# Kernel optimization log

Hardware: AMD Instinct MI355X
Metric: run time of the kernel (lower is better)

## Reference

```python
import jax, jax.numpy as jnp
import numpy as np

BN_EPS = 1e-5
B, N, D, E, L, VOCAB = 256, 256, 256, 262144, 5, 16
V = B * N


def batch_norm(h, g, b):
    # BatchNorm1d in training mode: biased batch stats over the node axis
    mu = jnp.mean(h, axis=0)
    var = jnp.mean((h - mu) ** 2, axis=0)
    return (h - mu) * jax.lax.rsqrt(var + BN_EPS) * g + b


def setup_inputs() -> dict:
    key = jax.random.key(0)
    ks = jax.random.split(key, 10)
    return {
        "x": jax.random.normal(ks[0], (B, N + 1, D), jnp.float32),
        "edge_weight": jax.random.uniform(ks[1], (E,), jnp.float32),
        "bond_emb": 0.02 * jax.random.normal(ks[2], (L, 3, VOCAB, D), jnp.float32),
        "W1": 0.02 * jax.random.normal(ks[3], (L, D, 2 * D), jnp.float32),
        "b1": jnp.zeros((L, 2 * D), jnp.float32),
        "bn1_g": jnp.ones((L, 2 * D), jnp.float32),
        "bn1_b": jnp.zeros((L, 2 * D), jnp.float32),
        "W2": 0.02 * jax.random.normal(ks[4], (L, 2 * D, D), jnp.float32),
        "b2": jnp.zeros((L, D), jnp.float32),
        "bn2_g": jnp.ones((L, D), jnp.float32),
        "bn2_b": jnp.zeros((L, D), jnp.float32),
        "eps_param": jnp.zeros((L,), jnp.float32),
        "x_mask": jnp.ones((B, N), jnp.int32),
        "edge_index": jax.random.randint(ks[5], (2, E), 0, V, jnp.int32),
        "edge_attr": jax.random.randint(ks[6], (E, 3), 0, VOCAB, jnp.int32),
    }


def reference(x, edge_weight, bond_emb, W1, b1, bn1_g, bn1_b, W2, b2,
              bn2_g, bn2_b, eps_param, x_mask, edge_index, edge_attr):
    res = x
    # mask is all-ones -> x[x_mask] equals the flattened [B*N, D] node tensor
    h = x[:, 1:, :].reshape(-1, D)
    mask = x_mask.reshape(-1).astype(x.dtype)[:, None]

    # add_self_loops: append (i, i) for every node; self-loop attr = [5, 7, 0]
    sl = jnp.arange(V, dtype=edge_index.dtype)
    src = jnp.concatenate([edge_index[0], sl])
    dst = jnp.concatenate([edge_index[1], sl])
    ea = jnp.concatenate(
        [edge_attr, jnp.broadcast_to(jnp.array([5, 7, 0], edge_attr.dtype), (V, 3))], axis=0)
    ew = jnp.concatenate([edge_weight, jnp.ones((V,), edge_weight.dtype)])

    for i in range(L):
        # BondEncoder: sum of per-feature embedding lookups -> [E+V, D]
        eemb = (bond_emb[i, 0][ea[:, 0]] + bond_emb[i, 1][ea[:, 1]]
                + bond_emb[i, 2][ea[:, 2]])
        msg = jax.nn.relu(h[src] + eemb) * ew[:, None]       # gather + relu
        aggr = jax.ops.segment_sum(msg, dst, num_segments=V)  # scatter-add
        z = (1.0 + eps_param[i]) * h + aggr
        z = batch_norm(z @ W1[i] + b1[i], bn1_g[i], bn1_b[i])
        z = jax.nn.relu(z) @ W2[i] + b2[i]
        z = batch_norm(z, bn2_g[i], bn2_b[i])                 # GNNBlock norm
        if i != L - 1:                                        # last_act
            z = jax.nn.relu(z)
        h = z                                                  # drop_ratio=0

    rep = h * mask  # x_zeros[x_mask] = node_representation (JK='last')
    return res.at[:, 1:, :].add(rep.reshape(res.shape[0], -1, D))
```

## Files before the change

kernel.cpp:

```cpp
#include <hip/hip_runtime.h>

#define E_EDGES 262144
#define V_NODES 65536
#define D_DIM   256

typedef short bf16x8 __attribute__((ext_vector_type(8)));
typedef float f32x4  __attribute__((ext_vector_type(4)));

__device__ __forceinline__ unsigned short f2bf(float f) {
  union { float f; unsigned u; } x; x.f = f;
  unsigned r = x.u + 0x7FFFu + ((x.u >> 16) & 1u);
  return (unsigned short)(r >> 16);
}
__device__ __forceinline__ float bf2f(unsigned short h) {
  union { unsigned u; float f; } x; x.u = ((unsigned)h) << 16;
  return x.f;
}
__device__ __forceinline__ void async16(const void* g, void* l) {
  __builtin_amdgcn_global_load_lds(
      (const __attribute__((address_space(1))) unsigned*)g,
      (__attribute__((address_space(3))) unsigned*)l, 16, 0, 0);
}

__global__ __launch_bounds__(256) void convert_weights_kernel(
    const float* __restrict__ W1, const float* __restrict__ W2,
    unsigned short* __restrict__ W1T, unsigned short* __restrict__ W2T) {
  int idx = blockIdx.x * 256 + threadIdx.x;
  {
    int k = idx & 255, n = (idx >> 8) & 511, i = idx >> 17;
    W1T[idx] = f2bf(W1[((size_t)(i * 256 + k)) * 512 + n]);
  }
  {
    int k = idx & 511, n = (idx >> 9) & 255, i = idx >> 17;
    W2T[idx] = f2bf(W2[((size_t)(i * 512 + k)) * 256 + n]);
  }
}

__global__ void hist_kernel(const int* __restrict__ ei, int* __restrict__ counts) {
  int e = blockIdx.x * 256 + threadIdx.x;
  int d = (e < E_EDGES) ? ei[E_EDGES + e] : (e - E_EDGES);
  atomicAdd(&counts[d], 1);
}
__global__ void scan1_kernel(const int* __restrict__ counts, int* __restrict__ indptr,
                             int* __restrict__ bsums) {
  __shared__ int s[256];
  int t = threadIdx.x, b = blockIdx.x;
  int v = counts[b * 256 + t];
  s[t] = v; __syncthreads();
  for (int off = 1; off < 256; off <<= 1) {
    int add = (t >= off) ? s[t - off] : 0;
    __syncthreads();
    s[t] += add;
    __syncthreads();
  }
  indptr[b * 256 + t] = s[t] - v;
  if (t == 255) bsums[b] = s[255];
}
__global__ void scan2_kernel(const int* __restrict__ bsums, int* __restrict__ boff) {
  __shared__ int s[256];
  int t = threadIdx.x;
  int v = bsums[t];
  s[t] = v; __syncthreads();
  for (int off = 1; off < 256; off <<= 1) {
    int add = (t >= off) ? s[t - off] : 0;
    __syncthreads();
    s[t] += add;
    __syncthreads();
  }
  boff[t] = s[t] - v;
}
__global__ void scan3_kernel(int* __restrict__ indptr, const int* __restrict__ boff) {
  int t = threadIdx.x, b = blockIdx.x;
  indptr[b * 256 + t] += boff[b];
  if (b == 0 && t == 0) indptr[V_NODES] = E_EDGES + V_NODES;
}
__global__ void scatter_kernel(const int* __restrict__ ei, const int* __restrict__ indptr,
                               int* __restrict__ fill, int* __restrict__ csr_eid) {
  int e = blockIdx.x * 256 + threadIdx.x;
  int d = (e < E_EDGES) ? ei[E_EDGES + e] : (e - E_EDGES);
  int pos = indptr[d] + atomicAdd(&fill[d], 1);
  csr_eid[pos] = e;
}

template <bool L0>
__device__ __forceinline__ void load_hnorm(int node, int c0, const float* __restrict__ x,
                                           const unsigned short* __restrict__ hprev,
                                           const float* sc, const float* sh, float* out) {
  if (L0) {
    const float* p = x + ((size_t)((node >> 8) * 257 + (node & 255) + 1)) * 256 + c0;
    float4 tv = *(const float4*)p;
    out[0] = tv.x; out[1] = tv.y; out[2] = tv.z; out[3] = tv.w;
  } else {
    ushort4 tv = *(const ushort4*)(hprev + (size_t)node * 256 + c0);
    out[0] = fmaxf(bf2f(tv.x) * sc[0] + sh[0], 0.f);
    out[1] = fmaxf(bf2f(tv.y) * sc[1] + sh[1], 0.f);
    out[2] = fmaxf(bf2f(tv.z) * sc[2] + sh[2], 0.f);
    out[3] = fmaxf(bf2f(tv.w) * sc[3] + sh[3], 0.f);
  }
}

template <bool L0>
__global__ __launch_bounds__(256) void msg_kernel(
    const float* __restrict__ x, const unsigned short* __restrict__ hprev,
    const float* __restrict__ scale2, const float* __restrict__ shift2,
    const int* __restrict__ indptr, const int* __restrict__ csr_eid,
    const int* __restrict__ ei, const int* __restrict__ ea, const float* __restrict__ ew,
    const float* __restrict__ bemb, const float* __restrict__ eps_param, int layer,
    float* __restrict__ aggr_f) {
  int wid = threadIdx.x >> 6;
  int lane = threadIdx.x & 63;
  int v = blockIdx.x * 4 + wid;
  int c0 = lane * 4;
  float ep = 1.0f + eps_param[layer];

  float sc[4], sh[4];
  if (!L0) {
#pragma unroll
    for (int j = 0; j < 4; ++j) { sc[j] = scale2[c0 + j]; sh[j] = shift2[c0 + j]; }
  }

  float hv[4];
  load_hnorm<L0>(v, c0, x, hprev, sc, sh, hv);
  float acc[4] = { ep * hv[0], ep * hv[1], ep * hv[2], ep * hv[3] };

  int beg = indptr[v], end = indptr[v + 1];
  for (int p = beg; p < end; ++p) {
    int eid = csr_eid[p];
    int s, a0, a1, a2; float w;
    if (eid < E_EDGES) {
      s = ei[eid];
      a0 = ea[eid * 3]; a1 = ea[eid * 3 + 1]; a2 = ea[eid * 3 + 2];
      w = ew[eid];
    } else {
      s = eid - E_EDGES; a0 = 5; a1 = 7; a2 = 0; w = 1.0f;
    }
    float hs[4];
    load_hnorm<L0>(s, c0, x, hprev, sc, sh, hs);
    float4 e0 = *(const float4*)(bemb + (size_t)(0 * 16 + a0) * 256 + c0);
    float4 e1 = *(const float4*)(bemb + (size_t)(1 * 16 + a1) * 256 + c0);
    float4 e2 = *(const float4*)(bemb + (size_t)(2 * 16 + a2) * 256 + c0);
    acc[0] += fmaxf(hs[0] + e0.x + e1.x + e2.x, 0.f) * w;
    acc[1] += fmaxf(hs[1] + e0.y + e1.y + e2.y, 0.f) * w;
    acc[2] += fmaxf(hs[2] + e0.z + e1.z + e2.z, 0.f) * w;
    acc[3] += fmaxf(hs[3] + e0.w + e1.w + e2.w, 0.f) * w;
  }
  float4 o; o.x = acc[0]; o.y = acc[1]; o.z = acc[2]; o.w = acc[3];
  *(float4*)(aggr_f + (size_t)v * 256 + c0) = o;
}

__global__ __launch_bounds__(256) void colsum_kernel(const float* __restrict__ aggr_f,
                                                     float* __restrict__ colsum) {
  int t = threadIdx.x;
  size_t base = (size_t)blockIdx.x * 64 * 256 + t;
  float s = 0.f;
#pragma unroll
  for (int r = 0; r < 64; ++r) s += aggr_f[base + (size_t)r * 256];
  atomicAdd(&colsum[t], s);
}

__global__ __launch_bounds__(256) void center_kernel(const float* __restrict__ aggr_f,
                                                     const float* __restrict__ colsum,
                                                     unsigned short* __restrict__ aggr_c) {
  size_t i = ((size_t)blockIdx.x * 256 + threadIdx.x) * 4;
  int c = (int)(i & 255);
  float4 v = *(const float4*)(aggr_f + i);
  const float inv = 1.0f / 65536.0f;
  ushort4 o;
  o.x = f2bf(v.x - colsum[c + 0] * inv);
  o.y = f2bf(v.y - colsum[c + 1] * inv);
  o.z = f2bf(v.z - colsum[c + 2] * inv);
  o.w = f2bf(v.w - colsum[c + 3] * inv);
  *(ushort4*)(aggr_c + i) = o;
}

template <int K, int N>
__global__ __launch_bounds__(256) void gemm_kernel(
    const unsigned short* __restrict__ A, const unsigned short* __restrict__ BT,
    const float* __restrict__ bias, unsigned short* __restrict__ C,
    float* __restrict__ sumP, float* __restrict__ sqP) {
  __shared__ char lds[16384];
  const int t = threadIdx.x;
  const int lane = t & 63;
  const int wid = t >> 6;
  const int waveM = wid >> 1, waveN = wid & 1;
  const int rowBase = blockIdx.x * 128;
  const int colBase = blockIdx.y * 128;
  const int kw = lane >> 4;
  const int l15 = lane & 15;

  f32x4 acc[4][4];
#pragma unroll
  for (int m = 0; m < 4; ++m)
#pragma unroll
    for (int n = 0; n < 4; ++n) acc[m][n] = (f32x4){0.f, 0.f, 0.f, 0.f};

  for (int k0 = 0; k0 < K; k0 += 32) {
#pragma unroll
    for (int c = 0; c < 2; ++c) {
      int row = c * 64 + (t >> 2);
      int gslot = (t & 3) ^ ((row >> 1) & 3);
      const unsigned short* ga = A + (size_t)(rowBase + row) * K + k0 + gslot * 8;
      async16(ga, lds + c * 4096 + wid * 1024);
      const unsigned short* gb = BT + (size_t)(colBase + row) * K + k0 + gslot * 8;
      async16(gb, lds + 8192 + c * 4096 + wid * 1024);
    }
    __syncthreads();

    bf16x8 af[4], bfr[4];
#pragma unroll
    for (int f = 0; f < 4; ++f) {
      int rA = waveM * 64 + f * 16 + l15;
      af[f] = *(const bf16x8*)(lds + rA * 64 + ((kw ^ ((rA >> 1) & 3)) * 16));
      int rB = waveN * 64 + f * 16 + l15;
      bfr[f] = *(const bf16x8*)(lds + 8192 + rB * 64 + ((kw ^ ((rB >> 1) & 3)) * 16));
    }
#pragma unroll
    for (int m = 0; m < 4; ++m)
#pragma unroll
      for (int n = 0; n < 4; ++n)
        acc[m][n] = __builtin_amdgcn_mfma_f32_16x16x32_bf16(af[m], bfr[n], acc[m][n], 0, 0, 0);
    __syncthreads();
  }

  const int cB = colBase + waveN * 64;
  const int rB0 = rowBase + waveM * 64;
#pragma unroll
  for (int n = 0; n < 4; ++n) {
    int col = cB + n * 16 + l15;
    float bcol = bias[col];
    float psum = 0.f, psq = 0.f;
#pragma unroll
    for (int m = 0; m < 4; ++m) {
#pragma unroll
      for (int r = 0; r < 4; ++r) {
        float val = acc[m][n][r] + bcol;
        int row = rB0 + m * 16 + kw * 4 + r;
        C[(size_t)row * N + col] = f2bf(val);
        psum += val; psq += val * val;
      }
    }
    psum += __shfl_xor(psum, 16); psum += __shfl_xor(psum, 32);
    psq  += __shfl_xor(psq, 16);  psq  += __shfl_xor(psq, 32);
    if (kw == 0) {
      int prow = blockIdx.x * 2 + waveM;
      sumP[(size_t)prow * N + col] = psum;
      sqP[(size_t)prow * N + col] = psq;
    }
  }
}

__global__ void finalize_kernel(const float* __restrict__ sumP, const float* __restrict__ sqP,
                                const float* __restrict__ g, const float* __restrict__ b,
                                float* __restrict__ scale, float* __restrict__ shift, int N) {
  __shared__ float ls[256], lq[256];
  int col = blockIdx.x, t = threadIdx.x;
  float s = 0.f, q = 0.f;
  for (int r = t; r < 1024; r += 256) {
    s += sumP[(size_t)r * N + col];
    q += sqP[(size_t)r * N + col];
  }
  ls[t] = s; lq[t] = q; __syncthreads();
  for (int off = 128; off > 0; off >>= 1) {
    if (t < off) { ls[t] += ls[t + off]; lq[t] += lq[t + off]; }
    __syncthreads();
  }
  if (t == 0) {
    float inv = 1.0f / 65536.0f;
    float mu = ls[0] * inv;
    float var = lq[0] * inv - mu * mu;
    float sc = g[col] * rsqrtf(var + 1e-5f);
    scale[col] = sc;
    shift[col] = b[col] - mu * sc;
  }
}

__global__ __launch_bounds__(256) void apply_bn_relu_kernel(
    unsigned short* __restrict__ z, const float* __restrict__ scale,
    const float* __restrict__ shift) {
  size_t i = ((size_t)blockIdx.x * 256 + threadIdx.x) * 8;
  int col = (int)(i & 511);
  ushort4 a = *(const ushort4*)(z + i);
  ushort4 b = *(const ushort4*)(z + i + 4);
  float f0 = fmaxf(bf2f(a.x) * scale[col + 0] + shift[col + 0], 0.f);
  float f1 = fmaxf(bf2f(a.y) * scale[col + 1] + shift[col + 1], 0.f);
  float f2 = fmaxf(bf2f(a.z) * scale[col + 2] + shift[col + 2], 0.f);
  float f3 = fmaxf(bf2f(a.w) * scale[col + 3] + shift[col + 3], 0.f);
  float f4 = fmaxf(bf2f(b.x) * scale[col + 4] + shift[col + 4], 0.f);
  float f5 = fmaxf(bf2f(b.y) * scale[col + 5] + shift[col + 5], 0.f);
  float f6 = fmaxf(bf2f(b.z) * scale[col + 6] + shift[col + 6], 0.f);
  float f7 = fmaxf(bf2f(b.w) * scale[col + 7] + shift[col + 7], 0.f);
  ushort4 oa, ob;
  oa.x = f2bf(f0); oa.y = f2bf(f1); oa.z = f2bf(f2); oa.w = f2bf(f3);
  ob.x = f2bf(f4); ob.y = f2bf(f5); ob.z = f2bf(f6); ob.w = f2bf(f7);
  *(ushort4*)(z + i) = oa;
  *(ushort4*)(z + i + 4) = ob;
}

__global__ void final_out_kernel(const float* __restrict__ x, const unsigned short* __restrict__ z2,
                                 const float* __restrict__ scale2, const float* __restrict__ shift2,
                                 const int* __restrict__ xmask, float* __restrict__ out) {
  int row = blockIdx.x;
  int b = blockIdx.y;
  int lane = threadIdx.x;
  size_t off = ((size_t)b * 257 + row) * 256 + lane * 4;
  float4 xv = *(const float4*)(x + off);
  if (row > 0) {
    int v = b * 256 + (row - 1);
    float m = (float)xmask[v];
    ushort4 tv = *(const ushort4*)(z2 + (size_t)v * 256 + lane * 4);
    int c = lane * 4;
    xv.x += m * (bf2f(tv.x) * scale2[c + 0] + shift2[c + 0]);
    xv.y += m * (bf2f(tv.y) * scale2[c + 1] + shift2[c + 1]);
    xv.z += m * (bf2f(tv.z) * scale2[c + 2] + shift2[c + 2]);
    xv.w += m * (bf2f(tv.w) * scale2[c + 3] + shift2[c + 3]);
  }
  *(float4*)(out + off) = xv;
}

extern "C" void kernel_launch(void* const* d_in, const int* in_sizes, int n_in,
                              void* d_out, int out_size, void* d_ws, size_t ws_size,
                              hipStream_t stream) {
  const float* x    = (const float*)d_in[0];
  const float* ew   = (const float*)d_in[1];
  const float* bemb = (const float*)d_in[2];
  const float* W1   = (const float*)d_in[3];
  const float* b1   = (const float*)d_in[4];
  const float* g1   = (const float*)d_in[5];
  const float* bb1  = (const float*)d_in[6];
  const float* W2   = (const float*)d_in[7];
  const float* b2   = (const float*)d_in[8];
  const float* g2   = (const float*)d_in[9];
  const float* bb2  = (const float*)d_in[10];
  const float* eps  = (const float*)d_in[11];
  const int* xmask  = (const int*)d_in[12];
  const int* ei     = (const int*)d_in[13];
  const int* ea     = (const int*)d_in[14];
  float* out = (float*)d_out;

  char* ws = (char*)d_ws;
  size_t off = 0;
  auto alloc = [&](size_t bytes) {
    char* p = ws + off;
    off += (bytes + 255) & ~(size_t)255;
    return p;
  };
  unsigned short* W1T = (unsigned short*)alloc(5ull * 512 * 256 * 2);
  unsigned short* W2T = (unsigned short*)alloc(5ull * 256 * 512 * 2);
  int* counts = (int*)alloc(65536ull * 4);
  int* fill   = (int*)alloc(65536ull * 4);
  int* indptr = (int*)alloc(65537ull * 4);
  int* bsums  = (int*)alloc(256 * 4);
  int* boff   = (int*)alloc(256 * 4);
  int* csr    = (int*)alloc(327680ull * 4);
  float* scale1 = (float*)alloc(512 * 4);
  float* shift1 = (float*)alloc(512 * 4);
  float* scale2 = (float*)alloc(256 * 4);
  float* shift2 = (float*)alloc(256 * 4);
  float* colsum = (float*)alloc(256 * 4);
  float* sumP = (float*)alloc(1024ull * 512 * 4);
  float* sqP  = (float*)alloc(1024ull * 512 * 4);
  float* aggr_f = (float*)alloc(65536ull * 256 * 4);
  unsigned short* aggr_c = (unsigned short*)alloc(65536ull * 256 * 2);
  unsigned short* z1   = (unsigned short*)alloc(65536ull * 512 * 2);
  unsigned short* z2   = (unsigned short*)alloc(65536ull * 256 * 2);
  (void)ws_size; (void)in_sizes; (void)n_in; (void)out_size;

  hipMemsetAsync(counts, 0, 65536ull * 4, stream);
  hipMemsetAsync(fill, 0, 65536ull * 4, stream);

  convert_weights_kernel<<<2560, 256, 0, stream>>>(W1, W2, W1T, W2T);
  hist_kernel<<<1280, 256, 0, stream>>>(ei, counts);
  scan1_kernel<<<256, 256, 0, stream>>>(counts, indptr, bsums);
  scan2_kernel<<<1, 256, 0, stream>>>(bsums, boff);
  scan3_kernel<<<256, 256, 0, stream>>>(indptr, boff);
  scatter_kernel<<<1280, 256, 0, stream>>>(ei, indptr, fill, csr);

  for (int i = 0; i < 5; ++i) {
    const float* bemb_l = bemb + (size_t)i * 3 * 16 * 256;
    if (i == 0)
      msg_kernel<true><<<16384, 256, 0, stream>>>(x, (const unsigned short*)nullptr, nullptr, nullptr,
                                                  indptr, csr, ei, ea, ew, bemb_l, eps, i, aggr_f);
    else
      msg_kernel<false><<<16384, 256, 0, stream>>>(x, z2, scale2, shift2,
                                                   indptr, csr, ei, ea, ew, bemb_l, eps, i, aggr_f);
    hipMemsetAsync(colsum, 0, 256 * 4, stream);
    colsum_kernel<<<1024, 256, 0, stream>>>(aggr_f, colsum);
    center_kernel<<<16384, 256, 0, stream>>>(aggr_f, colsum, aggr_c);
    gemm_kernel<256, 512><<<dim3(512, 4), 256, 0, stream>>>(
        aggr_c, W1T + (size_t)i * 512 * 256, b1 + i * 512, z1, sumP, sqP);
    finalize_kernel<<<512, 256, 0, stream>>>(sumP, sqP, g1 + i * 512, bb1 + i * 512,
                                             scale1, shift1, 512);
    apply_bn_relu_kernel<<<16384, 256, 0, stream>>>(z1, scale1, shift1);
    gemm_kernel<512, 256><<<dim3(512, 2), 256, 0, stream>>>(
        z1, W2T + (size_t)i * 256 * 512, b2 + i * 256, z2, sumP, sqP);
    finalize_kernel<<<256, 256, 0, stream>>>(sumP, sqP, g2 + i * 256, bb2 + i * 256,
                                             scale2, shift2, 256);
  }
  final_out_kernel<<<dim3(257, 256), 64, 0, stream>>>(x, z2, scale2, shift2, xmask, out);
}
```

Measured before the change: 1.453 ms.

## Fuse BN1+ReLU into second GEMM A-load, center z2 in fp32, prefetch edges

The separate BN1+ReLU pass over z1 is removed. The second GEMM now applies the scale/shift and ReLU while staging its A tile into LDS, so it no longer reads and writes z1 an extra time. The second GEMM writes fp32 output into the reused aggr_f buffer, and a new center kernel subtracts the batch mean before converting to bf16, which improves precision but adds a pass over fp32 data. The message kernel also software-prefetches the next edge's metadata to hide gather latency.

```diff
diff --git a/kernel.cpp b/kernel.cpp
--- a/kernel.cpp
+++ b/kernel.cpp
@@ -124,25 +124,32 @@
   float acc[4] = { ep * hv[0], ep * hv[1], ep * hv[2], ep * hv[3] };
 
   int beg = indptr[v], end = indptr[v + 1];
+  int eid = csr_eid[beg];
+  int s, a0, a1, a2; float w;
+  if (eid < E_EDGES) {
+    s = ei[eid]; a0 = ea[eid * 3]; a1 = ea[eid * 3 + 1]; a2 = ea[eid * 3 + 2]; w = ew[eid];
+  } else { s = eid - E_EDGES; a0 = 5; a1 = 7; a2 = 0; w = 1.0f; }
+
   for (int p = beg; p < end; ++p) {
-    int eid = csr_eid[p];
-    int s, a0, a1, a2; float w;
-    if (eid < E_EDGES) {
-      s = ei[eid];
-      a0 = ea[eid * 3]; a1 = ea[eid * 3 + 1]; a2 = ea[eid * 3 + 2];
-      w = ew[eid];
-    } else {
-      s = eid - E_EDGES; a0 = 5; a1 = 7; a2 = 0; w = 1.0f;
-    }
     float hs[4];
     load_hnorm<L0>(s, c0, x, hprev, sc, sh, hs);
-    float4 e0 = *(const float4*)(bemb + (size_t)(0 * 16 + a0) * 256 + c0);
-    float4 e1 = *(const float4*)(bemb + (size_t)(1 * 16 + a1) * 256 + c0);
-    float4 e2 = *(const float4*)(bemb + (size_t)(2 * 16 + a2) * 256 + c0);
-    acc[0] += fmaxf(hs[0] + e0.x + e1.x + e2.x, 0.f) * w;
-    acc[1] += fmaxf(hs[1] + e0.y + e1.y + e2.y, 0.f) * w;
-    acc[2] += fmaxf(hs[2] + e0.z + e1.z + e2.z, 0.f) * w;
-    acc[3] += fmaxf(hs[3] + e0.w + e1.w + e2.w, 0.f) * w;
+    float4 e0 = *(const float4*)(bemb + (size_t)(a0) * 256 + c0);
+    float4 e1 = *(const float4*)(bemb + (size_t)(16 + a1) * 256 + c0);
+    float4 e2 = *(const float4*)(bemb + (size_t)(32 + a2) * 256 + c0);
+    float wc = w;
+
+    if (p + 1 < end) {
+      int eidn = csr_eid[p + 1];
+      if (eidn < E_EDGES) {
+        s = ei[eidn]; a0 = ea[eidn * 3]; a1 = ea[eidn * 3 + 1]; a2 = ea[eidn * 3 + 2];
+        w = ew[eidn];
+      } else { s = eidn - E_EDGES; a0 = 5; a1 = 7; a2 = 0; w = 1.0f; }
+    }
+
+    acc[0] += fmaxf(hs[0] + e0.x + e1.x + e2.x, 0.f) * wc;
+    acc[1] += fmaxf(hs[1] + e0.y + e1.y + e2.y, 0.f) * wc;
+    acc[2] += fmaxf(hs[2] + e0.z + e1.z + e2.z, 0.f) * wc;
+    acc[3] += fmaxf(hs[3] + e0.w + e1.w + e2.w, 0.f) * wc;
   }
   float4 o; o.x = acc[0]; o.y = acc[1]; o.z = acc[2]; o.w = acc[3];
   *(float4*)(aggr_f + (size_t)v * 256 + c0) = o;
@@ -249,6 +256,104 @@
   }
 }
 
+__global__ __launch_bounds__(256) void gemm2_kernel(
+    const unsigned short* __restrict__ A , const unsigned short* __restrict__ BT,
+    const float* __restrict__ scA, const float* __restrict__ shA,
+    const float* __restrict__ bias, float* __restrict__ C ,
+    float* __restrict__ sumP, float* __restrict__ sqP) {
+  const int K = 512, N = 256;
+  __shared__ char lds[16384];
+  const int t = threadIdx.x;
+  const int lane = t & 63;
+  const int wid = t >> 6;
+  const int waveM = wid >> 1, waveN = wid & 1;
+  const int rowBase = blockIdx.x * 128;
+  const int colBase = blockIdx.y * 128;
+  const int kw = lane >> 4;
+  const int l15 = lane & 15;
+
+  f32x4 acc[4][4];
+#pragma unroll
+  for (int m = 0; m < 4; ++m)
+#pragma unroll
+    for (int n = 0; n < 4; ++n) acc[m][n] = (f32x4){0.f, 0.f, 0.f, 0.f};
+
+  for (int k0 = 0; k0 < K; k0 += 32) {
+#pragma unroll
+    for (int c = 0; c < 2; ++c) {
+      int row = c * 64 + (t >> 2);
+      int gslot = (t & 3) ^ ((row >> 1) & 3);
+      const unsigned short* gb = BT + (size_t)(colBase + row) * K + k0 + gslot * 8;
+      async16(gb, lds + 8192 + c * 4096 + wid * 1024);
+    }
+#pragma unroll
+    for (int c = 0; c < 2; ++c) {
+      int row = c * 64 + (t >> 2);
+      int gslot = (t & 3) ^ ((row >> 1) & 3);
+      int kk = k0 + gslot * 8;
+      const unsigned short* ga = A + (size_t)(rowBase + row) * K + kk;
+      ushort4 a0 = *(const ushort4*)ga;
+      ushort4 a1 = *(const ushort4*)(ga + 4);
+      float4 s0 = *(const float4*)(scA + kk);
+      float4 s1 = *(const float4*)(scA + kk + 4);
+      float4 h0 = *(const float4*)(shA + kk);
+      float4 h1 = *(const float4*)(shA + kk + 4);
+      bf16x8 o;
+      o[0] = (short)f2bf(fmaxf(bf2f(a0.x) * s0.x + h0.x, 0.f));
+      o[1] = (short)f2bf(fmaxf(bf2f(a0.y) * s0.y + h0.y, 0.f));
+      o[2] = (short)f2bf(fmaxf(bf2f(a0.z) * s0.z + h0.z, 0.f));
+      o[3] = (short)f2bf(fmaxf(bf2f(a0.w) * s0.w + h0.w, 0.f));
+      o[4] = (short)f2bf(fmaxf(bf2f(a1.x) * s1.x + h1.x, 0.f));
+      o[5] = (short)f2bf(fmaxf(bf2f(a1.y) * s1.y + h1.y, 0.f));
+      o[6] = (short)f2bf(fmaxf(bf2f(a1.z) * s1.z + h1.z, 0.f));
+      o[7] = (short)f2bf(fmaxf(bf2f(a1.w) * s1.w + h1.w, 0.f));
+      *(bf16x8*)(lds + c * 4096 + wid * 1024 + (t & 63) * 16) = o;
+    }
+    __syncthreads();
+
+    bf16x8 af[4], bfr[4];
+#pragma unroll
+    for (int f = 0; f < 4; ++f) {
+      int rA = waveM * 64 + f * 16 + l15;
+      af[f] = *(const bf16x8*)(lds + rA * 64 + ((kw ^ ((rA >> 1) & 3)) * 16));
+      int rB = waveN * 64 + f * 16 + l15;
+      bfr[f] = *(const bf16x8*)(lds + 8192 + rB * 64 + ((kw ^ ((rB >> 1) & 3)) * 16));
+    }
+#pragma unroll
+    for (int m = 0; m < 4; ++m)
+#pragma unroll
+      for (int n = 0; n < 4; ++n)
+        acc[m][n] = __builtin_amdgcn_mfma_f32_16x16x32_bf16(af[m], bfr[n], acc[m][n], 0, 0, 0);
+    __syncthreads();
+  }
+
+  const int cB = colBase + waveN * 64;
+  const int rB0 = rowBase + waveM * 64;
+#pragma unroll
+  for (int n = 0; n < 4; ++n) {
+    int col = cB + n * 16 + l15;
+    float bcol = bias[col];
+    float psum = 0.f, psq = 0.f;
+#pragma unroll
+    for (int m = 0; m < 4; ++m) {
+#pragma unroll
+      for (int r = 0; r < 4; ++r) {
+        float val = acc[m][n][r] + bcol;
+        int row = rB0 + m * 16 + kw * 4 + r;
+        C[(size_t)row * N + col] = val;
+        psum += val; psq += val * val;
+      }
+    }
+    psum += __shfl_xor(psum, 16); psum += __shfl_xor(psum, 32);
+    psq  += __shfl_xor(psq, 16);  psq  += __shfl_xor(psq, 32);
+    if (kw == 0) {
+      int prow = blockIdx.x * 2 + waveM;
+      sumP[(size_t)prow * N + col] = psum;
+      sqP[(size_t)prow * N + col] = psq;
+    }
+  }
+}
+
 __global__ void finalize_kernel(const float* __restrict__ sumP, const float* __restrict__ sqP,
                                 const float* __restrict__ g, const float* __restrict__ b,
                                 float* __restrict__ scale, float* __restrict__ shift, int N) {
@@ -274,29 +379,47 @@
   }
 }
 
-__global__ __launch_bounds__(256) void apply_bn_relu_kernel(
-    unsigned short* __restrict__ z, const float* __restrict__ scale,
-    const float* __restrict__ shift) {
-  size_t i = ((size_t)blockIdx.x * 256 + threadIdx.x) * 8;
-  int col = (int)(i & 511);
-  ushort4 a = *(const ushort4*)(z + i);
-  ushort4 b = *(const ushort4*)(z + i + 4);
-  float f0 = fmaxf(bf2f(a.x) * scale[col + 0] + shift[col + 0], 0.f);
-  float f1 = fmaxf(bf2f(a.y) * scale[col + 1] + shift[col + 1], 0.f);
-  float f2 = fmaxf(bf2f(a.z) * scale[col + 2] + shift[col + 2], 0.f);
-  float f3 = fmaxf(bf2f(a.w) * scale[col + 3] + shift[col + 3], 0.f);
-  float f4 = fmaxf(bf2f(b.x) * scale[col + 4] + shift[col + 4], 0.f);
-  float f5 = fmaxf(bf2f(b.y) * scale[col + 5] + shift[col + 5], 0.f);
-  float f6 = fmaxf(bf2f(b.z) * scale[col + 6] + shift[col + 6], 0.f);
-  float f7 = fmaxf(bf2f(b.w) * scale[col + 7] + shift[col + 7], 0.f);
-  ushort4 oa, ob;
-  oa.x = f2bf(f0); oa.y = f2bf(f1); oa.z = f2bf(f2); oa.w = f2bf(f3);
-  ob.x = f2bf(f4); ob.y = f2bf(f5); ob.z = f2bf(f6); ob.w = f2bf(f7);
-  *(ushort4*)(z + i) = oa;
-  *(ushort4*)(z + i + 4) = ob;
-}
-
-__global__ void final_out_kernel(const float* __restrict__ x, const unsigned short* __restrict__ z2,
+__global__ void finalize2_kernel(const float* __restrict__ sumP, const float* __restrict__ sqP,
+                                 const float* __restrict__ g, const float* __restrict__ b,
+                                 float* __restrict__ scale, float* __restrict__ shift,
+                                 float* __restrict__ mu_out, int N) {
+  __shared__ float ls[256], lq[256];
+  int col = blockIdx.x, t = threadIdx.x;
+  float s = 0.f, q = 0.f;
+  for (int r = t; r < 1024; r += 256) {
+    s += sumP[(size_t)r * N + col];
+    q += sqP[(size_t)r * N + col];
+  }
+  ls[t] = s; lq[t] = q; __syncthreads();
+  for (int off = 128; off > 0; off >>= 1) {
+    if (t < off) { ls[t] += ls[t + off]; lq[t] += lq[t + off]; }
+    __syncthreads();
+  }
+  if (t == 0) {
+    float inv = 1.0f / 65536.0f;
+    float mu = ls[0] * inv;
+    float var = lq[0] * inv - mu * mu;
+    scale[col] = g[col] * rsqrtf(var + 1e-5f);
+    shift[col] = b[col];
+    mu_out[col] = mu;
+  }
+}
+
+__global__ __launch_bounds__(256) void center2_kernel(const float* __restrict__ z2f,
+                                                      const float* __restrict__ mu2,
+                                                      unsigned short* __restrict__ z2c) {
+  size_t i = ((size_t)blockIdx.x * 256 + threadIdx.x) * 4;
+  int c = (int)(i & 255);
+  float4 v = *(const float4*)(z2f + i);
+  ushort4 o;
+  o.x = f2bf(v.x - mu2[c + 0]);
+  o.y = f2bf(v.y - mu2[c + 1]);
+  o.z = f2bf(v.z - mu2[c + 2]);
+  o.w = f2bf(v.w - mu2[c + 3]);
+  *(ushort4*)(z2c + i) = o;
+}
+
+__global__ void final_out_kernel(const float* __restrict__ x, const unsigned short* __restrict__ z2c,
                                  const float* __restrict__ scale2, const float* __restrict__ shift2,
                                  const int* __restrict__ xmask, float* __restrict__ out) {
   int row = blockIdx.x;
@@ -307,7 +430,7 @@
   if (row > 0) {
     int v = b * 256 + (row - 1);
     float m = (float)xmask[v];
-    ushort4 tv = *(const ushort4*)(z2 + (size_t)v * 256 + lane * 4);
+    ushort4 tv = *(const ushort4*)(z2c + (size_t)v * 256 + lane * 4);
     int c = lane * 4;
     xv.x += m * (bf2f(tv.x) * scale2[c + 0] + shift2[c + 0]);
     xv.y += m * (bf2f(tv.y) * scale2[c + 1] + shift2[c + 1]);
@@ -357,12 +480,13 @@
   float* scale2 = (float*)alloc(256 * 4);
   float* shift2 = (float*)alloc(256 * 4);
   float* colsum = (float*)alloc(256 * 4);
+  float* mu2    = (float*)alloc(256 * 4);
   float* sumP = (float*)alloc(1024ull * 512 * 4);
   float* sqP  = (float*)alloc(1024ull * 512 * 4);
   float* aggr_f = (float*)alloc(65536ull * 256 * 4);
   unsigned short* aggr_c = (unsigned short*)alloc(65536ull * 256 * 2);
   unsigned short* z1   = (unsigned short*)alloc(65536ull * 512 * 2);
-  unsigned short* z2   = (unsigned short*)alloc(65536ull * 256 * 2);
+  unsigned short* z2c  = (unsigned short*)alloc(65536ull * 256 * 2);
   (void)ws_size; (void)in_sizes; (void)n_in; (void)out_size;
 
   hipMemsetAsync(counts, 0, 65536ull * 4, stream);
@@ -381,7 +505,7 @@
       msg_kernel<true><<<16384, 256, 0, stream>>>(x, (const unsigned short*)nullptr, nullptr, nullptr,
                                                   indptr, csr, ei, ea, ew, bemb_l, eps, i, aggr_f);
     else
-      msg_kernel<false><<<16384, 256, 0, stream>>>(x, z2, scale2, shift2,
+      msg_kernel<false><<<16384, 256, 0, stream>>>(x, z2c, scale2, shift2,
                                                    indptr, csr, ei, ea, ew, bemb_l, eps, i, aggr_f);
     hipMemsetAsync(colsum, 0, 256 * 4, stream);
     colsum_kernel<<<1024, 256, 0, stream>>>(aggr_f, colsum);
@@ -390,11 +514,11 @@
         aggr_c, W1T + (size_t)i * 512 * 256, b1 + i * 512, z1, sumP, sqP);
     finalize_kernel<<<512, 256, 0, stream>>>(sumP, sqP, g1 + i * 512, bb1 + i * 512,
                                              scale1, shift1, 512);
-    apply_bn_relu_kernel<<<16384, 256, 0, stream>>>(z1, scale1, shift1);
-    gemm_kernel<512, 256><<<dim3(512, 2), 256, 0, stream>>>(
-        z1, W2T + (size_t)i * 256 * 512, b2 + i * 256, z2, sumP, sqP);
-    finalize_kernel<<<256, 256, 0, stream>>>(sumP, sqP, g2 + i * 256, bb2 + i * 256,
-                                             scale2, shift2, 256);
-  }
-  final_out_kernel<<<dim3(257, 256), 64, 0, stream>>>(x, z2, scale2, shift2, xmask, out);
-}
+    gemm2_kernel<<<dim3(512, 2), 256, 0, stream>>>(
+        z1, W2T + (size_t)i * 256 * 512, scale1, shift1, b2 + i * 256, aggr_f, sumP, sqP);
+    finalize2_kernel<<<256, 256, 0, stream>>>(sumP, sqP, g2 + i * 256, bb2 + i * 256,
+                                              scale2, shift2, mu2, 256);
+    center2_kernel<<<16384, 256, 0, stream>>>(aggr_f, mu2, z2c);
+  }
+  final_out_kernel<<<dim3(257, 256), 64, 0, stream>>>(x, z2c, scale2, shift2, xmask, out);
+}
```

Measured after the change: 1.458 ms. No clear change (+0.4%).
